# Performance work log

Measured on AMD Instinct MI355X. Metric: run time of the kernel, lower is better.

The kernel has to match this reference:

```python
import jax, jax.numpy as jnp
import numpy as np
from jax.ops import segment_sum, segment_max

N = 100000   # nodes
E = 1600000  # edges
B = 256      # graphs
H = 128      # hidden_channels
F_IN = 4     # input_size
EPS = 1e-5


def _graph_norm(x, w, b, ms, batch):
    # PyG GraphNorm: out = w * (x - ms*mean_g) / sqrt(var_g + eps) + b
    cnt = jnp.maximum(segment_sum(jnp.ones((x.shape[0],), x.dtype), batch, num_segments=B), 1.0)
    mean = segment_sum(x, batch, num_segments=B) / cnt[:, None]
    out = x - mean[batch] * ms
    var = segment_sum(out * out, batch, num_segments=B) / cnt[:, None]
    return w * out / jnp.sqrt(var + EPS)[batch] + b


def _gcn(x, W, b, src, dst):
    # GCNConv with self-loops and symmetric normalization (src/dst already include self-loops)
    h = x @ W                                              # [N, H]
    deg = segment_sum(jnp.ones_like(src, dtype=h.dtype), dst, num_segments=N)
    dinv = jax.lax.rsqrt(jnp.maximum(deg, 1.0))
    norm = dinv[src] * dinv[dst]                           # [E+N]
    return segment_sum(norm[:, None] * h[src], dst, num_segments=N) + b


def _seg_softmax(gate, batch):
    gmax = segment_max(gate, batch, num_segments=B)
    e = jnp.exp(gate - gmax[batch])
    den = segment_sum(e, batch, num_segments=B)
    return e / den[batch]


def setup_inputs() -> dict:
    key = jax.random.key(0)
    ks = jax.random.split(key, 16)
    x = jax.random.normal(ks[0], (N, F_IN), jnp.float32)
    edge_index = jax.random.randint(ks[1], (2, E), 0, N, dtype=jnp.int64)
    batch = jnp.sort(jax.random.randint(ks[2], (N,), 0, B, dtype=jnp.int64))
    r = lambda k, shp, fan: jax.random.normal(k, shp, jnp.float32) / np.sqrt(fan)
    inp = {
        "x": x, "edge_index": edge_index, "batch": batch,
        "W1": r(ks[3], (F_IN, H), F_IN), "b1": jnp.zeros((H,), jnp.float32),
        "W2": r(ks[4], (H, H), H), "b2": jnp.zeros((H,), jnp.float32),
        "W3": r(ks[5], (H, H), H), "b3": jnp.zeros((H,), jnp.float32),
        "gn0_w": jnp.ones((F_IN,), jnp.float32), "gn0_b": jnp.zeros((F_IN,), jnp.float32), "gn0_ms": jnp.ones((F_IN,), jnp.float32),
        "gn1_w": jnp.ones((H,), jnp.float32), "gn1_b": jnp.zeros((H,), jnp.float32), "gn1_ms": jnp.ones((H,), jnp.float32),
        "gn2_w": jnp.ones((H,), jnp.float32), "gn2_b": jnp.zeros((H,), jnp.float32), "gn2_ms": jnp.ones((H,), jnp.float32),
        "gn3_w": jnp.ones((H,), jnp.float32), "gn3_b": jnp.zeros((H,), jnp.float32), "gn3_ms": jnp.ones((H,), jnp.float32),
        "g1": r(ks[6], (H, H), H), "gb1": jnp.zeros((H,), jnp.float32),
        "g2": r(ks[7], (H, H), H), "gb2": jnp.zeros((H,), jnp.float32),
        "g3": r(ks[8], (H, 1), H), "gb3": jnp.zeros((1,), jnp.float32),
        "l1": r(ks[9], (H, H), H), "lb1": jnp.zeros((H,), jnp.float32),
        "l2": r(ks[10], (H, H), H), "lb2": jnp.zeros((H,), jnp.float32),
        "l3": r(ks[11], (H, 1), H), "lb3": jnp.zeros((1,), jnp.float32),
    }
    return inp


def reference(x, edge_index, batch, W1, b1, W2, b2, W3, b3,
              gn0_w, gn0_b, gn0_ms, gn1_w, gn1_b, gn1_ms,
              gn2_w, gn2_b, gn2_ms, gn3_w, gn3_b, gn3_ms,
              g1, gb1, g2, gb2, g3, gb3,
              l1, lb1, l2, lb2, l3, lb3):
    loop = jnp.arange(N, dtype=edge_index.dtype)
    src = jnp.concatenate([edge_index[0], loop])
    dst = jnp.concatenate([edge_index[1], loop])

    h = _graph_norm(x, gn0_w, gn0_b, gn0_ms, batch)
    h = _gcn(h, W1, b1, src, dst)
    h = jax.nn.relu(_graph_norm(h, gn1_w, gn1_b, gn1_ms, batch))
    h = _gcn(h, W2, b2, src, dst)
    h = jax.nn.relu(_graph_norm(h, gn2_w, gn2_b, gn2_ms, batch))
    h = _gcn(h, W3, b3, src, dst)
    h = _graph_norm(h, gn3_w, gn3_b, gn3_ms, batch)

    # GlobalAttention: gate_nn -> scalar gate per node, segment softmax, weighted sum
    g = jax.nn.relu(h @ g1 + gb1)
    g = jax.nn.relu(g @ g2 + gb2)
    gate = g @ g3 + gb3                                   # [N, 1]
    attn = _seg_softmax(gate, batch)                      # [N, 1]
    pooled = segment_sum(attn * h, batch, num_segments=B) # [B, H]

    o = jax.nn.relu(pooled @ l1 + lb1)
    o = jax.nn.relu(o @ l2 + lb2)
    return o @ l3 + lb3                                   # [B, 1]
```

## Files before the change

kernel.cpp:

```cpp
#include <hip/hip_runtime.h>
#include <hip/hip_bf16.h>

#define NN 100000
#define NE 1600000
#define NB 256
#define HD 128
#define EPS 1e-5f
#define NBUK 1563
#define SLOTB 1536
#define EPB 8192
#define NCHK 8

typedef __attribute__((ext_vector_type(8))) short bf16x8v;
typedef __attribute__((ext_vector_type(4))) float f32x4v;

__device__ __forceinline__ float rd_dyn(const void* p, int i, int fflag) {
    if (fflag) {
        unsigned short u = ((const unsigned short*)p)[i];
        return __uint_as_float(((unsigned)u) << 16);
    }
    return ((const float*)p)[i];
}

__device__ __forceinline__ int rd_idx(const int* p, int k, int iflag) {
    return iflag ? p[k] : p[2 * k];
}

__device__ __forceinline__ unsigned short f2bf(float v) {
    __hip_bfloat16 b = __float2bfloat16(v);
    return *(unsigned short*)&b;
}

__device__ __forceinline__ float bflo(unsigned u) { return __uint_as_float(u << 16); }
__device__ __forceinline__ float bfhi(unsigned u) { return __uint_as_float(u & 0xFFFF0000u); }
__device__ __forceinline__ unsigned packbf(float a, float b) {
    return (unsigned)f2bf(a) | ((unsigned)f2bf(b) << 16);
}

__global__ void k_mark7(unsigned short* __restrict__ out, int n) {
    int i = blockIdx.x * blockDim.x + threadIdx.x;
    if (i < n) out[i] = 0x40E0;
}

__global__ void k_init(const unsigned* __restrict__ w, int* __restrict__ flags) {
    if (threadIdx.x == 0 && blockIdx.x == 0) {
        flags[0] = 0;
        flags[1] = (w[0] == 0x3F803F80u) ? 1 : 0;
    }
}

__global__ void k_detect(const int* __restrict__ w, int* __restrict__ iflag, int n) {
    int i = blockIdx.x * blockDim.x + threadIdx.x;
    if (i < n && (i & 1) && w[i] != 0) atomicOr(iflag, 1);
}

struct CvtArgs {
    const void* p[30];
    int n[30];
    int off[30];
};
__global__ void k_cvtf_all(CvtArgs a, float* __restrict__ out, const int* __restrict__ fflagp) {
    int j = blockIdx.y;
    int i = blockIdx.x * blockDim.x + threadIdx.x;
    if (i >= a.n[j]) return;
    out[a.off[j] + i] = rd_dyn(a.p[j], i, *fflagp);
}

__global__ void k_transp(const float* __restrict__ P, int o0, int o1, int o2, int o3,
                         unsigned short* __restrict__ WT) {
    int mat = blockIdx.y;
    int off = mat == 0 ? o0 : mat == 1 ? o1 : mat == 2 ? o2 : o3;
    int i = blockIdx.x * 256 + threadIdx.x;
    int nidx = i >> 7, k = i & 127;
    WT[mat * 16384 + nidx * 128 + k] = f2bf(P[off + k * 128 + nidx]);
}

__global__ void k_start(const int* __restrict__ batch, const int* __restrict__ iflagp,
                        int* __restrict__ start, int* __restrict__ batch32,
                        int* __restrict__ bcur, int n) {
    int i = blockIdx.x * blockDim.x + threadIdx.x;
    if (i >= n) return;
    if (i < NBUK) bcur[i] = i * SLOTB;
    int ifl = *iflagp;
    int b = rd_idx(batch, i, ifl); b = b < 0 ? 0 : (b > NB - 1 ? NB - 1 : b);
    batch32[i] = b;
    int bp;
    if (i == 0) bp = -1;
    else { bp = rd_idx(batch, i - 1, ifl); bp = bp < 0 ? 0 : (bp > NB - 1 ? NB - 1 : bp); }
    for (int g = bp + 1; g <= b; ++g) start[g] = i;
    if (i == n - 1) { for (int g = b + 1; g <= NB; ++g) start[g] = n; }
}

__global__ __launch_bounds__(256) void k_bfill(const int* __restrict__ ei,
                                               const int* __restrict__ iflagp,
                                               int* __restrict__ bcur,
                                               unsigned* __restrict__ bkte, int e) {
    __shared__ int lh[NBUK];
    __shared__ int lbase[NBUK];
    int ifl = *iflagp;
    for (int b = threadIdx.x; b < NBUK; b += 256) lh[b] = 0;
    __syncthreads();
    int s0 = blockIdx.x * EPB;
    int s1 = s0 + EPB; if (s1 > e) s1 = e;
    for (int i = s0 + threadIdx.x; i < s1; i += 256) {
        int d = rd_idx(ei, NE + i, ifl);
        int s = rd_idx(ei, i, ifl);
        if ((unsigned)d < (unsigned)NN && (unsigned)s < (unsigned)NN)
            atomicAdd(&lh[d >> 6], 1);
    }
    __syncthreads();
    for (int b = threadIdx.x; b < NBUK; b += 256) {
        int c = lh[b];
        if (c) { lbase[b] = atomicAdd(&bcur[b], c); lh[b] = 0; }
    }
    __syncthreads();
    for (int i = s0 + threadIdx.x; i < s1; i += 256) {
        int d = rd_idx(ei, NE + i, ifl);
        int s = rd_idx(ei, i, ifl);
        if ((unsigned)d < (unsigned)NN && (unsigned)s < (unsigned)NN) {
            int b = d >> 6;
            int li = atomicAdd(&lh[b], 1);
            bkte[lbase[b] + li] = ((unsigned)s << 6) | (unsigned)(d & 63);
        }
    }
}

__global__ __launch_bounds__(256) void k_csrfin(const unsigned* __restrict__ bkte,
                                                const int* __restrict__ bcur,
                                                int* __restrict__ rowptr,
                                                int* __restrict__ cnt,
                                                float* __restrict__ dinv,
                                                int* __restrict__ esrc) {
    __shared__ int lc[64];
    __shared__ int lcur[64];
    int b = blockIdx.x, t = threadIdx.x;
    int base = b * 64;
    if (t < 64) lc[t] = 0;
    __syncthreads();
    int r0 = b * SLOTB, r1 = bcur[b];
    for (int j = r0 + t; j < r1; j += 256)
        atomicAdd(&lc[(int)(bkte[j] & 63u)], 1);
    __syncthreads();
    if (t < 64) {
        int v = lc[t];
        int inc = v;
#pragma unroll
        for (int off = 1; off < 64; off <<= 1) {
            int nv = __shfl_up(inc, off, 64);
            if (t >= off) inc += nv;
        }
        int ex = r0 + inc - v;
        lcur[t] = ex;
        int node = base + t;
        if (node < NN) {
            rowptr[node] = ex;
            cnt[node] = v;
            dinv[node] = rsqrtf((float)(v + 1));
        }
    }
    __syncthreads();
    for (int j = r0 + t; j < r1; j += 256) {
        unsigned p = bkte[j];
        int slot = atomicAdd(&lcur[p & 63u], 1);
        esrc[slot] = (int)(p >> 6);
    }
}

__global__ __launch_bounds__(64) void k_gn4(const void* __restrict__ x,
                                            const float* __restrict__ w,
                                            const float* __restrict__ bb,
                                            const float* __restrict__ ms,
                                            const int* __restrict__ start,
                                            const int* __restrict__ fflagp,
                                            float* __restrict__ out) {
    int g = blockIdx.x;
    int s0 = start[g], s1 = start[g + 1];
    if (s1 <= s0) return;
    int ff = *fflagp;
    float cnt = (float)(s1 - s0);
    int t = threadIdx.x;
    int c = t & 3, p = t >> 2;
    __shared__ float reds[64], redq[64];
    float s = 0.f, q = 0.f;
    for (int n = s0 + p; n < s1; n += 16) {
        float v = rd_dyn(x, n * 4 + c, ff);
        s += v; q = fmaf(v, v, q);
    }
    reds[t] = s; redq[t] = q; __syncthreads();
    for (int off = 8; off >= 1; off >>= 1) {
        if (p < off) { reds[t] += reds[t + 4 * off]; redq[t] += redq[t + 4 * off]; }
        __syncthreads();
    }
    float mean = reds[c] / cnt;
    float sq = redq[c] / cnt;
    float sub = mean * ms[c];
    float var = sq - 2.f * sub * mean + sub * sub;
    float scale = w[c] * rsqrtf(var + EPS);
    float bias = bb[c];
    for (int n = s0 + p; n < s1; n += 16) {
        float d = rd_dyn(x, n * 4 + c, ff) - sub;
        out[n * 4 + c] = scale * d + bias;
    }
}

__global__ __launch_bounds__(256) void k_gnstats_part(const unsigned* __restrict__ Xu,
                                                      const int* __restrict__ start,
                                                      float* __restrict__ PS,
                                                      float* __restrict__ PQ) {
    int g = blockIdx.x, k = blockIdx.y;
    int s0 = start[g], s1 = start[g + 1];
    int len = (s1 - s0 + NCHK - 1) / NCHK;
    int c0 = s0 + k * len, c1 = c0 + len; if (c1 > s1) c1 = s1;
    int t = threadIdx.x;
    int cp = t & 63, p = t >> 6;
    __shared__ float r0s[256], r1s[256], r0q[256], r1q[256];
    float s0a = 0.f, s1a = 0.f, q0a = 0.f, q1a = 0.f;
    for (int n = c0 + p; n < c1; n += 4) {
        unsigned u = Xu[n * 64 + cp];
        float lo = bflo(u), hi = bfhi(u);
        s0a += lo; q0a = fmaf(lo, lo, q0a);
        s1a += hi; q1a = fmaf(hi, hi, q1a);
    }
    r0s[t] = s0a; r1s[t] = s1a; r0q[t] = q0a; r1q[t] = q1a;
    __syncthreads();
    if (p == 0) {
        float a0 = r0s[cp] + r0s[64 + cp] + r0s[128 + cp] + r0s[192 + cp];
        float a1 = r1s[cp] + r1s[64 + cp] + r1s[128 + cp] + r1s[192 + cp];
        float b0 = r0q[cp] + r0q[64 + cp] + r0q[128 + cp] + r0q[192 + cp];
        float b1 = r1q[cp] + r1q[64 + cp] + r1q[128 + cp] + r1q[192 + cp];
        int bidx = (g * NCHK + k) * 128;
        PS[bidx + 2 * cp] = a0; PS[bidx + 2 * cp + 1] = a1;
        PQ[bidx + 2 * cp] = b0; PQ[bidx + 2 * cp + 1] = b1;
    }
}

__global__ __launch_bounds__(128) void k_gnstats_final(const float* __restrict__ PS,
                                                       const float* __restrict__ PQ,
                                                       const float* __restrict__ w,
                                                       const float* __restrict__ ms,
                                                       const int* __restrict__ start,
                                                       float* __restrict__ SUB,
                                                       float* __restrict__ SCALE) {
    int g = blockIdx.x, c = threadIdx.x;
    int n = start[g + 1] - start[g];
    if (n <= 0) return;
    float cnt = (float)n;
    float s = 0.f, q = 0.f;
#pragma unroll
    for (int k = 0; k < NCHK; ++k) {
        s += PS[(g * NCHK + k) * 128 + c];
        q += PQ[(g * NCHK + k) * 128 + c];
    }
    float mean = s / cnt;
    float sq = q / cnt;
    float sub = mean * ms[c];
    float var = sq - 2.f * sub * mean + sub * sub;
    SUB[g * 128 + c] = sub;
    SCALE[g * 128 + c] = w[c] * rsqrtf(var + EPS);
}

__global__ __launch_bounds__(256) void k_gather4gemm(const int* __restrict__ rowptr,
                                                     const int* __restrict__ cnt,
                                                     const int* __restrict__ esrc,
                                                     const float* __restrict__ dinv,
                                                     const float* __restrict__ h0,
                                                     const float* __restrict__ W1,
                                                     const float* __restrict__ b1,
                                                     unsigned* __restrict__ Xu) {
    __shared__ float w1s[512];
    __shared__ float b1s[128];
    int tid = threadIdx.x;
    w1s[tid] = W1[tid];
    w1s[256 + tid] = W1[256 + tid];
    if (tid < 128) b1s[tid] = b1[tid];
    __syncthreads();
    int node = blockIdx.x * 4 + (tid >> 6);
    int lane = tid & 63;
    if (node >= NN) return;
    int ch = lane & 3;
    int r0 = rowptr[node], r1 = r0 + cnt[node];
    float acc = 0.f;
    for (int j = r0 + (lane >> 2); j < r1; j += 16) {
        int s = esrc[j];
        acc += dinv[s] * h0[s * 4 + ch];
    }
#pragma unroll
    for (int mask = 4; mask <= 32; mask <<= 1)
        acc += __shfl_xor(acc, mask, 64);
    float dd = dinv[node];
    float z = dd * acc + dd * dd * h0[node * 4 + ch];
    float za = __shfl(z, 0, 64), zb = __shfl(z, 1, 64);
    float zc = __shfl(z, 2, 64), zd = __shfl(z, 3, 64);
    int c0 = 2 * lane, c1 = 2 * lane + 1;
    float v0 = za * w1s[c0] + zb * w1s[128 + c0] + zc * w1s[256 + c0] + zd * w1s[384 + c0] + b1s[c0];
    float v1 = za * w1s[c1] + zb * w1s[128 + c1] + zc * w1s[256 + c1] + zd * w1s[384 + c1] + b1s[c1];
    Xu[node * 64 + lane] = packbf(v0, v1);
}

__global__ __launch_bounds__(256) void k_gemm_mfma_bf(const unsigned* __restrict__ Xu,
                                                      const int* __restrict__ batch32,
                                                      const float* __restrict__ SUB,
                                                      const float* __restrict__ SCALE,
                                                      const float* __restrict__ gnb,
                                                      int relu,
                                                      const unsigned short* __restrict__ WT,
                                                      const float* __restrict__ dinv,
                                                      unsigned short* __restrict__ out) {
    __shared__ unsigned short xs[16][136];
    int base = blockIdx.x * 16;
    int tid = threadIdx.x;
    for (int idx = tid; idx < 1024; idx += 256) {
        int r = idx >> 6, cp = idx & 63;
        int g = batch32[base + r];
        unsigned u = Xu[(base + r) * 64 + cp];
        float2 sub = ((const float2*)(SUB + g * 128))[cp];
        float2 sc  = ((const float2*)(SCALE + g * 128))[cp];
        float2 gb  = ((const float2*)gnb)[cp];
        float va = (bflo(u) - sub.x) * sc.x + gb.x;
        float vb = (bfhi(u) - sub.y) * sc.y + gb.y;
        if (relu) { va = fmaxf(va, 0.f); vb = fmaxf(vb, 0.f); }
        xs[r][2 * cp] = f2bf(va);
        xs[r][2 * cp + 1] = f2bf(vb);
    }
    __syncthreads();
    int wave = tid >> 6, lane = tid & 63;
    int m = lane & 15, quad = lane >> 4;
    f32x4v acc0 = {0.f, 0.f, 0.f, 0.f}, acc1 = {0.f, 0.f, 0.f, 0.f};
    int c0 = wave * 32 + m, c1 = c0 + 16;
#pragma unroll
    for (int kk = 0; kk < 4; ++kk) {
        int ko = kk * 32 + quad * 8;
        bf16x8v a  = *(const bf16x8v*)&xs[m][ko];
        bf16x8v b0 = *(const bf16x8v*)&WT[c0 * 128 + ko];
        bf16x8v b1 = *(const bf16x8v*)&WT[c1 * 128 + ko];
        acc0 = __builtin_amdgcn_mfma_f32_16x16x32_bf16(a, b0, acc0, 0, 0, 0);
        acc1 = __builtin_amdgcn_mfma_f32_16x16x32_bf16(a, b1, acc1, 0, 0, 0);
    }
#pragma unroll
    for (int reg = 0; reg < 4; ++reg) {
        int row = base + quad * 4 + reg;
        float dv = dinv[row];
        out[row * 128 + c0] = f2bf(dv * acc0[reg]);
        out[row * 128 + c1] = f2bf(dv * acc1[reg]);
    }
}

#define ACC4(u) do { \
    a0 += bflo((u).x); a1 += bfhi((u).x); \
    a2 += bflo((u).y); a3 += bfhi((u).y); \
    a4 += bflo((u).z); a5 += bfhi((u).z); \
    a6 += bflo((u).w); a7 += bfhi((u).w); } while (0)

__global__ __launch_bounds__(256) void k_gather_bf(const int* __restrict__ rowptr,
                                                   const int* __restrict__ cnt,
                                                   const int* __restrict__ esrc,
                                                   const float* __restrict__ dinv,
                                                   const unsigned* __restrict__ h,
                                                   const float* __restrict__ bias,
                                                   unsigned* __restrict__ Xu) {
    int node = blockIdx.x * 4 + (threadIdx.x >> 6);
    int lane = threadIdx.x & 63;
    if (node >= NN) return;
    int q = lane >> 4, s = lane & 15;
    int r0 = rowptr[node], r1 = r0 + cnt[node];
    const uint4* hp = (const uint4*)h;
    float a0 = 0.f, a1 = 0.f, a2 = 0.f, a3 = 0.f;
    float a4 = 0.f, a5 = 0.f, a6 = 0.f, a7 = 0.f;
    int j = r0 + q;
    for (; j + 12 < r1; j += 16) {
        int e0 = esrc[j], e1 = esrc[j + 4], e2 = esrc[j + 8], e3 = esrc[j + 12];
        uint4 u0 = hp[e0 * 16 + s];
        uint4 u1 = hp[e1 * 16 + s];
        uint4 u2 = hp[e2 * 16 + s];
        uint4 u3 = hp[e3 * 16 + s];
        ACC4(u0); ACC4(u1); ACC4(u2); ACC4(u3);
    }
    for (; j + 4 < r1; j += 8) {
        int e0 = esrc[j], e1 = esrc[j + 4];
        uint4 u0 = hp[e0 * 16 + s];
        uint4 u1 = hp[e1 * 16 + s];
        ACC4(u0); ACC4(u1);
    }
    for (; j < r1; j += 4) {
        int e0 = esrc[j];
        uint4 u0 = hp[e0 * 16 + s];
        ACC4(u0);
    }
    a0 += __shfl_xor(a0, 16, 64); a0 += __shfl_xor(a0, 32, 64);
    a1 += __shfl_xor(a1, 16, 64); a1 += __shfl_xor(a1, 32, 64);
    a2 += __shfl_xor(a2, 16, 64); a2 += __shfl_xor(a2, 32, 64);
    a3 += __shfl_xor(a3, 16, 64); a3 += __shfl_xor(a3, 32, 64);
    a4 += __shfl_xor(a4, 16, 64); a4 += __shfl_xor(a4, 32, 64);
    a5 += __shfl_xor(a5, 16, 64); a5 += __shfl_xor(a5, 32, 64);
    a6 += __shfl_xor(a6, 16, 64); a6 += __shfl_xor(a6, 32, 64);
    a7 += __shfl_xor(a7, 16, 64); a7 += __shfl_xor(a7, 32, 64);
    int cp = 4 * s + q;
    float ax = q == 0 ? a0 : q == 1 ? a2 : q == 2 ? a4 : a6;
    float ay = q == 0 ? a1 : q == 1 ? a3 : q == 2 ? a5 : a7;
    float dd = dinv[node];
    unsigned us = h[node * 64 + cp];
    float2 bb = ((const float2*)bias)[cp];
    float ox = dd * (ax + bflo(us)) + bb.x;
    float oy = dd * (ay + bfhi(us)) + bb.y;
    Xu[node * 64 + cp] = packbf(ox, oy);
}

__global__ __launch_bounds__(256) void k_gate_fused(const unsigned* __restrict__ Xu,
                                                    const int* __restrict__ batch32,
                                                    const float* __restrict__ SUB,
                                                    const float* __restrict__ SCALE,
                                                    const float* __restrict__ gnb,
                                                    const unsigned short* __restrict__ GT1,
                                                    const float* __restrict__ gb1,
                                                    const unsigned short* __restrict__ GT2,
                                                    const float* __restrict__ gb2,
                                                    const float* __restrict__ g3,
                                                    const float* __restrict__ gb3,
                                                    float* __restrict__ gate) {
    __shared__ unsigned short xs[16][136];
    __shared__ unsigned short t1[16][136];
    __shared__ float redw[64];
    int base = blockIdx.x * 16;
    int tid = threadIdx.x;
    for (int idx = tid; idx < 1024; idx += 256) {
        int r = idx >> 6, cp = idx & 63;
        int g = batch32[base + r];
        unsigned u = Xu[(base + r) * 64 + cp];
        float2 sub = ((const float2*)(SUB + g * 128))[cp];
        float2 sc  = ((const float2*)(SCALE + g * 128))[cp];
        float2 gb  = ((const float2*)gnb)[cp];
        xs[r][2 * cp] = f2bf((bflo(u) - sub.x) * sc.x + gb.x);
        xs[r][2 * cp + 1] = f2bf((bfhi(u) - sub.y) * sc.y + gb.y);
    }
    __syncthreads();
    int wave = tid >> 6, lane = tid & 63;
    int m = lane & 15, quad = lane >> 4;
    int c0 = wave * 32 + m, c1 = c0 + 16;
    f32x4v acc0 = {0.f, 0.f, 0.f, 0.f}, acc1 = {0.f, 0.f, 0.f, 0.f};
#pragma unroll
    for (int kk = 0; kk < 4; ++kk) {
        int ko = kk * 32 + quad * 8;
        bf16x8v a  = *(const bf16x8v*)&xs[m][ko];
        bf16x8v b0 = *(const bf16x8v*)&GT1[c0 * 128 + ko];
        bf16x8v b1 = *(const bf16x8v*)&GT1[c1 * 128 + ko];
        acc0 = __builtin_amdgcn_mfma_f32_16x16x32_bf16(a, b0, acc0, 0, 0, 0);
        acc1 = __builtin_amdgcn_mfma_f32_16x16x32_bf16(a, b1, acc1, 0, 0, 0);
    }
    float bj0 = gb1[c0], bj1 = gb1[c1];
#pragma unroll
    for (int reg = 0; reg < 4; ++reg) {
        int row = quad * 4 + reg;
        t1[row][c0] = f2bf(fmaxf(acc0[reg] + bj0, 0.f));
        t1[row][c1] = f2bf(fmaxf(acc1[reg] + bj1, 0.f));
    }
    __syncthreads();
    f32x4v d0 = {0.f, 0.f, 0.f, 0.f}, d1 = {0.f, 0.f, 0.f, 0.f};
#pragma unroll
    for (int kk = 0; kk < 4; ++kk) {
        int ko = kk * 32 + quad * 8;
        bf16x8v a  = *(const bf16x8v*)&t1[m][ko];
        bf16x8v b0 = *(const bf16x8v*)&GT2[c0 * 128 + ko];
        bf16x8v b1 = *(const bf16x8v*)&GT2[c1 * 128 + ko];
        d0 = __builtin_amdgcn_mfma_f32_16x16x32_bf16(a, b0, d0, 0, 0, 0);
        d1 = __builtin_amdgcn_mfma_f32_16x16x32_bf16(a, b1, d1, 0, 0, 0);
    }
    float g30 = g3[c0], g31 = g3[c1];
    float bk0 = gb2[c0], bk1 = gb2[c1];
    float contrib[4];
#pragma unroll
    for (int reg = 0; reg < 4; ++reg) {
        float v0 = fmaxf(d0[reg] + bk0, 0.f);
        float v1 = fmaxf(d1[reg] + bk1, 0.f);
        contrib[reg] = v0 * g30 + v1 * g31;
    }
#pragma unroll
    for (int mask = 1; mask <= 8; mask <<= 1) {
#pragma unroll
        for (int reg = 0; reg < 4; ++reg)
            contrib[reg] += __shfl_xor(contrib[reg], mask, 64);
    }
    if (m == 0) {
#pragma unroll
        for (int reg = 0; reg < 4; ++reg)
            redw[wave * 16 + quad * 4 + reg] = contrib[reg];
    }
    __syncthreads();
    if (tid < 16) {
        float s = redw[tid] + redw[16 + tid] + redw[32 + tid] + redw[48 + tid];
        gate[base + tid] = s + gb3[0];
    }
}

__global__ __launch_bounds__(256) void k_smstats(const float* __restrict__ gate,
                                                 const int* __restrict__ start,
                                                 float2* __restrict__ SM) {
    int g = blockIdx.x;
    int s0 = start[g], s1 = start[g + 1];
    int t = threadIdx.x;
    __shared__ float red[256];
    if (s1 <= s0) { if (t == 0) SM[g] = make_float2(0.f, 1.f); return; }
    float m = -1e30f;
    for (int i = s0 + t; i < s1; i += 256) m = fmaxf(m, gate[i]);
    red[t] = m; __syncthreads();
    for (int off = 128; off; off >>= 1) { if (t < off) red[t] = fmaxf(red[t], red[t + off]); __syncthreads(); }
    m = red[0]; __syncthreads();
    float s = 0.f;
    for (int i = s0 + t; i < s1; i += 256) s += expf(gate[i] - m);
    red[t] = s; __syncthreads();
    for (int off = 128; off; off >>= 1) { if (t < off) red[t] += red[t + off]; __syncthreads(); }
    if (t == 0) SM[g] = make_float2(m, red[0]);
}

__global__ __launch_bounds__(256) void k_pool_part(const unsigned* __restrict__ Xu,
                                                   const float* __restrict__ SUB,
                                                   const float* __restrict__ SCALE,
                                                   const float* __restrict__ gnb,
                                                   const float* __restrict__ gate,
                                                   const float2* __restrict__ SM,
                                                   const int* __restrict__ start,
                                                   float* __restrict__ PP) {
    int g = blockIdx.x, k = blockIdx.y;
    int s0 = start[g], s1 = start[g + 1];
    int len = (s1 - s0 + NCHK - 1) / NCHK;
    int c0 = s0 + k * len, c1 = c0 + len; if (c1 > s1) c1 = s1;
    int t = threadIdx.x, cp = t & 63, p = t >> 6;
    __shared__ float r0s[256], r1s[256];
    float2 sm = SM[g];
    float invden = 1.f / sm.y;
    float2 sub = ((const float2*)(SUB + g * 128))[cp];
    float2 sc  = ((const float2*)(SCALE + g * 128))[cp];
    float2 gb  = ((const float2*)gnb)[cp];
    float sa = 0.f, sb = 0.f;
    for (int n = c0 + p; n < c1; n += 4) {
        float a = expf(gate[n] - sm.x) * invden;
        unsigned u = Xu[n * 64 + cp];
        sa += a * ((bflo(u) - sub.x) * sc.x + gb.x);
        sb += a * ((bfhi(u) - sub.y) * sc.y + gb.y);
    }
    r0s[t] = sa; r1s[t] = sb; __syncthreads();
    if (p == 0) {
        int bidx = (g * NCHK + k) * 128;
        float2 o;
        o.x = r0s[cp] + r0s[64 + cp] + r0s[128 + cp] + r0s[192 + cp];
        o.y = r1s[cp] + r1s[64 + cp] + r1s[128 + cp] + r1s[192 + cp];
        ((float2*)(PP + bidx))[cp] = o;
    }
}

__global__ __launch_bounds__(128) void k_head(const float* __restrict__ PP,
                                              const float* __restrict__ l1, const float* __restrict__ lb1,
                                              const float* __restrict__ l2, const float* __restrict__ lb2,
                                              const float* __restrict__ l3, const float* __restrict__ lb3,
                                              const int* __restrict__ fflagp,
                                              void* __restrict__ out) {
    int g = blockIdx.x, t = threadIdx.x;
    __shared__ float p[128], o[128], red[128];
    float s = 0.f;
#pragma unroll
    for (int k = 0; k < NCHK; ++k) s += PP[(g * NCHK + k) * 128 + t];
    p[t] = s; __syncthreads();
    float a = 0.f;
    for (int k = 0; k < 128; ++k) a += p[k] * l1[k * 128 + t];
    a = fmaxf(a + lb1[t], 0.f);
    o[t] = a; __syncthreads();
    float b = 0.f;
    for (int k = 0; k < 128; ++k) b += o[k] * l2[k * 128 + t];
    b = fmaxf(b + lb2[t], 0.f);
    red[t] = b * l3[t]; __syncthreads();
    for (int off = 64; off; off >>= 1) { if (t < off) red[t] += red[t + off]; __syncthreads(); }
    if (t == 0) {
        float r = red[0] + lb3[0];
        if (*fflagp) ((__hip_bfloat16*)out)[g] = __float2bfloat16(r);
        else ((float*)out)[g] = r;
    }
}

extern "C" void kernel_launch(void* const* d_in, const int* in_sizes, int n_in,
                              void* d_out, int out_size, void* d_ws, size_t ws_size,
                              hipStream_t stream) {
    const void* x = d_in[0];
    const int* ei_raw = (const int*)d_in[1];
    const int* batch_raw = (const int*)d_in[2];
    (void)n_in; (void)out_size;

    char* ws = (char*)d_ws;
    size_t off = 0;
    auto alloc = [&](size_t bytes) -> void* {
        void* p = ws + off;
        off += (bytes + 255) & ~(size_t)255;
        return p;
    };
    unsigned* Xu  = (unsigned*)alloc((size_t)NN * HD * 2);
    float* Y      = (float*)alloc((size_t)NN * HD * 4);
    float* h0     = (float*)alloc((size_t)NN * 4 * 4);
    float* dinv   = (float*)alloc((size_t)NN * 4);
    float* gate   = (float*)alloc((size_t)NN * 4);
    int*   start  = (int*)alloc((size_t)(NB + 1) * 4);
    int*   batch32= (int*)alloc((size_t)NN * 4);
    float* P      = (float*)alloc((size_t)131072 * 4);
    unsigned short* WT = (unsigned short*)alloc((size_t)4 * 16384 * 2);
    float* SUB    = (float*)alloc((size_t)NB * HD * 4);
    float* SCALE  = (float*)alloc((size_t)NB * HD * 4);
    float* PS     = (float*)alloc((size_t)NB * NCHK * 128 * 4);
    float* PQ     = (float*)alloc((size_t)NB * NCHK * 128 * 4);
    float2* SM    = (float2*)alloc((size_t)NB * 8);
    int*   flags  = (int*)alloc(256);
    int*   rowptr = (int*)alloc((size_t)NN * 4);
    int*   cnt    = (int*)alloc((size_t)NN * 4);
    int*   esrc   = (int*)alloc((size_t)NBUK * SLOTB * 4);
    int*   bcur   = (int*)alloc((size_t)NBUK * 4);
    unsigned* bkte = (unsigned*)(Y + (size_t)NN * HD / 2);
    float* PP = PS;

    if (ws_size < off) {
        k_mark7<<<1, 256, 0, stream>>>((unsigned short*)d_out, NB);
        return;
    }

    int* iflag = flags;
    int* fflag = flags + 1;
    k_init<<<1, 64, 0, stream>>>((const unsigned*)d_in[12], flags);
    k_detect<<<(NN + 255) / 256, 256, 0, stream>>>(batch_raw, iflag, NN);

    CvtArgs ca;
    float* fp[33];
    int maxn = 1;
    {
        int poff = 0;
        for (int i = 3; i < 33; ++i) {
            int n = in_sizes[i];
            ca.p[i - 3] = d_in[i];
            ca.n[i - 3] = n;
            ca.off[i - 3] = poff;
            fp[i] = P + poff;
            poff += n;
            if (n > maxn) maxn = n;
        }
    }
    {
        dim3 grid((maxn + 255) / 256, 30);
        k_cvtf_all<<<grid, 256, 0, stream>>>(ca, P, fflag);
    }
    const float *W1 = fp[3], *b1 = fp[4], *b2 = fp[6], *b3 = fp[8];
    const float *gn0w = fp[9],  *gn0b = fp[10], *gn0m = fp[11];
    const float *gn1w = fp[12], *gn1b = fp[13], *gn1m = fp[14];
    const float *gn2w = fp[15], *gn2b = fp[16], *gn2m = fp[17];
    const float *gn3w = fp[18], *gn3b = fp[19], *gn3m = fp[20];
    const float *gb1 = fp[22], *gb2 = fp[24], *g3 = fp[25], *gb3 = fp[26];
    const float *l1 = fp[27], *lb1 = fp[28], *l2 = fp[29], *lb2 = fp[30], *l3 = fp[31], *lb3 = fp[32];

    {
        dim3 grid(64, 4);
        k_transp<<<grid, 256, 0, stream>>>(P, (int)(fp[5] - P), (int)(fp[7] - P),
                                           (int)(fp[21] - P), (int)(fp[23] - P), WT);
    }
    const unsigned short* WT2 = WT;
    const unsigned short* WT3 = WT + 16384;
    const unsigned short* GT1 = WT + 2 * 16384;
    const unsigned short* GT2 = WT + 3 * 16384;

    k_start<<<(NN + 255) / 256, 256, 0, stream>>>(batch_raw, iflag, start, batch32, bcur, NN);

    int ebg = (NE + EPB - 1) / EPB;
    k_bfill<<<ebg, 256, 0, stream>>>(ei_raw, iflag, bcur, bkte, NE);
    k_csrfin<<<NBUK, 256, 0, stream>>>(bkte, bcur, rowptr, cnt, dinv, esrc);

    k_gn4<<<NB, 64, 0, stream>>>(x, gn0w, gn0b, gn0m, start, fflag, h0);

    k_gather4gemm<<<(NN + 3) / 4, 256, 0, stream>>>(rowptr, cnt, esrc, dinv, h0, W1, b1, Xu);

    unsigned short* Yb = (unsigned short*)Y;
    dim3 sgrid(NB, NCHK);

    k_gnstats_part<<<sgrid, 256, 0, stream>>>(Xu, start, PS, PQ);
    k_gnstats_final<<<NB, 128, 0, stream>>>(PS, PQ, gn1w, gn1m, start, SUB, SCALE);
    k_gemm_mfma_bf<<<NN / 16, 256, 0, stream>>>(Xu, batch32, SUB, SCALE, gn1b, 1, WT2, dinv, Yb);
    k_gather_bf<<<(NN + 3) / 4, 256, 0, stream>>>(rowptr, cnt, esrc, dinv, (const unsigned*)Yb, b2, Xu);

    k_gnstats_part<<<sgrid, 256, 0, stream>>>(Xu, start, PS, PQ);
    k_gnstats_final<<<NB, 128, 0, stream>>>(PS, PQ, gn2w, gn2m, start, SUB, SCALE);
    k_gemm_mfma_bf<<<NN / 16, 256, 0, stream>>>(Xu, batch32, SUB, SCALE, gn2b, 1, WT3, dinv, Yb);
    k_gather_bf<<<(NN + 3) / 4, 256, 0, stream>>>(rowptr, cnt, esrc, dinv, (const unsigned*)Yb, b3, Xu);

    k_gnstats_part<<<sgrid, 256, 0, stream>>>(Xu, start, PS, PQ);
    k_gnstats_final<<<NB, 128, 0, stream>>>(PS, PQ, gn3w, gn3m, start, SUB, SCALE);
    k_gate_fused<<<NN / 16, 256, 0, stream>>>(Xu, batch32, SUB, SCALE, gn3b,
                                              GT1, gb1, GT2, gb2, g3, gb3, gate);
    k_smstats<<<NB, 256, 0, stream>>>(gate, start, SM);
    k_pool_part<<<sgrid, 256, 0, stream>>>(Xu, SUB, SCALE, gn3b, gate, SM, start, PP);
    k_head<<<NB, 128, 0, stream>>>(PP, l1, lb1, l2, lb2, l3, lb3, fflag, d_out);
}
```

Measured before the change: 540.1 us.

## Merge small setup kernels, vectorize GraphNorm-0 and layer-1 gather, fuse softmax into pooling

Folds the flag-init kernel into the detect kernel (with a memset) and the weight transpose into the parameter-convert kernel. The pooling kernel now also computes the per-graph softmax max and denominator, so the separate stats kernel goes away; each chunk block recomputes those graph-wide stats redundantly. The input GraphNorm and the first gather switch to float4 per-node loads with one node per lane, and the GraphNorm block grows to 256 threads. The goal is fewer launches and better memory coalescing, at the cost of some duplicated reduction work.

```diff
diff --git a/kernel.cpp b/kernel.cpp
--- a/kernel.cpp
+++ b/kernel.cpp
@@ -42,37 +42,34 @@
     if (i < n) out[i] = 0x40E0;
 }
 
-__global__ void k_init(const unsigned* __restrict__ w, int* __restrict__ flags) {
-    if (threadIdx.x == 0 && blockIdx.x == 0) {
-        flags[0] = 0;
-        flags[1] = (w[0] == 0x3F803F80u) ? 1 : 0;
-    }
-}
-
-__global__ void k_detect(const int* __restrict__ w, int* __restrict__ iflag, int n) {
+__global__ void k_detect(const int* __restrict__ batch, const unsigned* __restrict__ w,
+                         int* __restrict__ flags, int n) {
     int i = blockIdx.x * blockDim.x + threadIdx.x;
-    if (i < n && (i & 1) && w[i] != 0) atomicOr(iflag, 1);
+    if (i == 0 && w[0] == 0x3F803F80u) atomicOr(&flags[1], 1);
+    if (i < n && (i & 1) && batch[i] != 0) atomicOr(&flags[0], 1);
 }
 
 struct CvtArgs {
     const void* p[30];
     int n[30];
     int off[30];
+    const void* wp[4];
 };
-__global__ void k_cvtf_all(CvtArgs a, float* __restrict__ out, const int* __restrict__ fflagp) {
+__global__ void k_cvtf_all(CvtArgs a, float* __restrict__ out,
+                           unsigned short* __restrict__ WT,
+                           const int* __restrict__ fflagp) {
     int j = blockIdx.y;
     int i = blockIdx.x * blockDim.x + threadIdx.x;
-    if (i >= a.n[j]) return;
-    out[a.off[j] + i] = rd_dyn(a.p[j], i, *fflagp);
-}
-
-__global__ void k_transp(const float* __restrict__ P, int o0, int o1, int o2, int o3,
-                         unsigned short* __restrict__ WT) {
-    int mat = blockIdx.y;
-    int off = mat == 0 ? o0 : mat == 1 ? o1 : mat == 2 ? o2 : o3;
-    int i = blockIdx.x * 256 + threadIdx.x;
-    int nidx = i >> 7, k = i & 127;
-    WT[mat * 16384 + nidx * 128 + k] = f2bf(P[off + k * 128 + nidx]);
+    int ff = *fflagp;
+    if (j < 30) {
+        if (i >= a.n[j]) return;
+        out[a.off[j] + i] = rd_dyn(a.p[j], i, ff);
+    } else {
+        int mat = j - 30;
+        if (i >= 16384) return;
+        int nidx = i >> 7, k = i & 127;
+        WT[mat * 16384 + nidx * 128 + k] = f2bf(rd_dyn(a.wp[mat], k * 128 + nidx, ff));
+    }
 }
 
 __global__ void k_start(const int* __restrict__ batch, const int* __restrict__ iflagp,
@@ -166,40 +163,72 @@
     }
 }
 
-__global__ __launch_bounds__(64) void k_gn4(const void* __restrict__ x,
-                                            const float* __restrict__ w,
-                                            const float* __restrict__ bb,
-                                            const float* __restrict__ ms,
-                                            const int* __restrict__ start,
-                                            const int* __restrict__ fflagp,
-                                            float* __restrict__ out) {
+__global__ __launch_bounds__(256) void k_gn4(const void* __restrict__ x,
+                                             const float* __restrict__ w,
+                                             const float* __restrict__ bb,
+                                             const float* __restrict__ ms,
+                                             const int* __restrict__ start,
+                                             const int* __restrict__ fflagp,
+                                             float* __restrict__ out) {
     int g = blockIdx.x;
     int s0 = start[g], s1 = start[g + 1];
     if (s1 <= s0) return;
     int ff = *fflagp;
     float cnt = (float)(s1 - s0);
     int t = threadIdx.x;
-    int c = t & 3, p = t >> 2;
-    __shared__ float reds[64], redq[64];
-    float s = 0.f, q = 0.f;
-    for (int n = s0 + p; n < s1; n += 16) {
-        float v = rd_dyn(x, n * 4 + c, ff);
-        s += v; q = fmaf(v, v, q);
-    }
-    reds[t] = s; redq[t] = q; __syncthreads();
-    for (int off = 8; off >= 1; off >>= 1) {
-        if (p < off) { reds[t] += reds[t + 4 * off]; redq[t] += redq[t + 4 * off]; }
+    __shared__ float4 rs[256], rq[256];
+    float sx = 0.f, sy = 0.f, sz = 0.f, sw = 0.f;
+    float qx = 0.f, qy = 0.f, qz = 0.f, qw = 0.f;
+    for (int n = s0 + t; n < s1; n += 256) {
+        float4 v;
+        if (ff) {
+            uint2 u = ((const uint2*)x)[n];
+            v.x = bflo(u.x); v.y = bfhi(u.x); v.z = bflo(u.y); v.w = bfhi(u.y);
+        } else {
+            v = ((const float4*)x)[n];
+        }
+        sx += v.x; sy += v.y; sz += v.z; sw += v.w;
+        qx = fmaf(v.x, v.x, qx); qy = fmaf(v.y, v.y, qy);
+        qz = fmaf(v.z, v.z, qz); qw = fmaf(v.w, v.w, qw);
+    }
+    rs[t] = make_float4(sx, sy, sz, sw);
+    rq[t] = make_float4(qx, qy, qz, qw);
+    __syncthreads();
+    for (int off = 128; off; off >>= 1) {
+        if (t < off) {
+            rs[t].x += rs[t + off].x; rs[t].y += rs[t + off].y;
+            rs[t].z += rs[t + off].z; rs[t].w += rs[t + off].w;
+            rq[t].x += rq[t + off].x; rq[t].y += rq[t + off].y;
+            rq[t].z += rq[t + off].z; rq[t].w += rq[t + off].w;
+        }
         __syncthreads();
     }
-    float mean = reds[c] / cnt;
-    float sq = redq[c] / cnt;
-    float sub = mean * ms[c];
-    float var = sq - 2.f * sub * mean + sub * sub;
-    float scale = w[c] * rsqrtf(var + EPS);
-    float bias = bb[c];
-    for (int n = s0 + p; n < s1; n += 16) {
-        float d = rd_dyn(x, n * 4 + c, ff) - sub;
-        out[n * 4 + c] = scale * d + bias;
+    float4 S = rs[0], Q = rq[0];
+    float4 wv = ((const float4*)w)[0];
+    float4 bv = ((const float4*)bb)[0];
+    float4 mv = ((const float4*)ms)[0];
+    float4 mean = make_float4(S.x / cnt, S.y / cnt, S.z / cnt, S.w / cnt);
+    float4 sub = make_float4(mean.x * mv.x, mean.y * mv.y, mean.z * mv.z, mean.w * mv.w);
+    float4 scale;
+    scale.x = wv.x * rsqrtf(Q.x / cnt - 2.f * sub.x * mean.x + sub.x * sub.x + EPS);
+    scale.y = wv.y * rsqrtf(Q.y / cnt - 2.f * sub.y * mean.y + sub.y * sub.y + EPS);
+    scale.z = wv.z * rsqrtf(Q.z / cnt - 2.f * sub.z * mean.z + sub.z * sub.z + EPS);
+    scale.w = wv.w * rsqrtf(Q.w / cnt - 2.f * sub.w * mean.w + sub.w * sub.w + EPS);
+    float4* op = (float4*)out;
+    for (int n = s0 + t; n < s1; n += 256) {
+        float4 v;
+        if (ff) {
+            uint2 u = ((const uint2*)x)[n];
+            v.x = bflo(u.x); v.y = bfhi(u.x); v.z = bflo(u.y); v.w = bfhi(u.y);
+        } else {
+            v = ((const float4*)x)[n];
+        }
+        float4 o;
+        o.x = scale.x * (v.x - sub.x) + bv.x;
+        o.y = scale.y * (v.y - sub.y) + bv.y;
+        o.z = scale.z * (v.z - sub.z) + bv.z;
+        o.w = scale.w * (v.w - sub.w) + bv.w;
+        op[n] = o;
     }
 }
 
@@ -277,20 +306,27 @@
     int node = blockIdx.x * 4 + (tid >> 6);
     int lane = tid & 63;
     if (node >= NN) return;
-    int ch = lane & 3;
     int r0 = rowptr[node], r1 = r0 + cnt[node];
-    float acc = 0.f;
-    for (int j = r0 + (lane >> 2); j < r1; j += 16) {
+    const float4* h4 = (const float4*)h0;
+    float ax = 0.f, ay = 0.f, az = 0.f, aw = 0.f;
+    for (int j = r0 + lane; j < r1; j += 64) {
         int s = esrc[j];
-        acc += dinv[s] * h0[s * 4 + ch];
-    }
-#pragma unroll
-    for (int mask = 4; mask <= 32; mask <<= 1)
-        acc += __shfl_xor(acc, mask, 64);
+        float dv = dinv[s];
+        float4 h = h4[s];
+        ax = fmaf(dv, h.x, ax); ay = fmaf(dv, h.y, ay);
+        az = fmaf(dv, h.z, az); aw = fmaf(dv, h.w, aw);
+    }
+#pragma unroll
+    for (int mask = 1; mask <= 32; mask <<= 1) {
+        ax += __shfl_xor(ax, mask, 64); ay += __shfl_xor(ay, mask, 64);
+        az += __shfl_xor(az, mask, 64); aw += __shfl_xor(aw, mask, 64);
+    }
     float dd = dinv[node];
-    float z = dd * acc + dd * dd * h0[node * 4 + ch];
-    float za = __shfl(z, 0, 64), zb = __shfl(z, 1, 64);
-    float zc = __shfl(z, 2, 64), zd = __shfl(z, 3, 64);
+    float4 hn = h4[node];
+    float za = dd * ax + dd * dd * hn.x;
+    float zb = dd * ay + dd * dd * hn.y;
+    float zc = dd * az + dd * dd * hn.z;
+    float zd = dd * aw + dd * dd * hn.w;
     int c0 = 2 * lane, c1 = 2 * lane + 1;
     float v0 = za * w1s[c0] + zb * w1s[128 + c0] + zc * w1s[256 + c0] + zd * w1s[384 + c0] + b1s[c0];
     float v1 = za * w1s[c1] + zb * w1s[128 + c1] + zc * w1s[256 + c1] + zd * w1s[384 + c1] + b1s[c1];
@@ -491,55 +527,51 @@
     }
 }
 
-__global__ __launch_bounds__(256) void k_smstats(const float* __restrict__ gate,
-                                                 const int* __restrict__ start,
-                                                 float2* __restrict__ SM) {
-    int g = blockIdx.x;
+__global__ __launch_bounds__(256) void k_smpool(const unsigned* __restrict__ Xu,
+                                                const float* __restrict__ SUB,
+                                                const float* __restrict__ SCALE,
+                                                const float* __restrict__ gnb,
+                                                const float* __restrict__ gate,
+                                                const int* __restrict__ start,
+                                                float* __restrict__ PP) {
+    int g = blockIdx.x, kk = blockIdx.y;
     int s0 = start[g], s1 = start[g + 1];
     int t = threadIdx.x;
     __shared__ float red[256];
-    if (s1 <= s0) { if (t == 0) SM[g] = make_float2(0.f, 1.f); return; }
+    __shared__ float r0s[256], r1s[256];
+    if (s1 <= s0) {
+        if (t < 64) {
+            int bidx = (g * NCHK + kk) * 128;
+            ((float2*)(PP + bidx))[t] = make_float2(0.f, 0.f);
+        }
+        return;
+    }
     float m = -1e30f;
     for (int i = s0 + t; i < s1; i += 256) m = fmaxf(m, gate[i]);
     red[t] = m; __syncthreads();
     for (int off = 128; off; off >>= 1) { if (t < off) red[t] = fmaxf(red[t], red[t + off]); __syncthreads(); }
     m = red[0]; __syncthreads();
-    float s = 0.f;
-    for (int i = s0 + t; i < s1; i += 256) s += expf(gate[i] - m);
-    red[t] = s; __syncthreads();
+    float sden = 0.f;
+    for (int i = s0 + t; i < s1; i += 256) sden += expf(gate[i] - m);
+    red[t] = sden; __syncthreads();
     for (int off = 128; off; off >>= 1) { if (t < off) red[t] += red[t + off]; __syncthreads(); }
-    if (t == 0) SM[g] = make_float2(m, red[0]);
-}
-
-__global__ __launch_bounds__(256) void k_pool_part(const unsigned* __restrict__ Xu,
-                                                   const float* __restrict__ SUB,
-                                                   const float* __restrict__ SCALE,
-                                                   const float* __restrict__ gnb,
-                                                   const float* __restrict__ gate,
-                                                   const float2* __restrict__ SM,
-                                                   const int* __restrict__ start,
-                                                   float* __restrict__ PP) {
-    int g = blockIdx.x, k = blockIdx.y;
-    int s0 = start[g], s1 = start[g + 1];
+    float invden = 1.f / red[0];
     int len = (s1 - s0 + NCHK - 1) / NCHK;
-    int c0 = s0 + k * len, c1 = c0 + len; if (c1 > s1) c1 = s1;
-    int t = threadIdx.x, cp = t & 63, p = t >> 6;
-    __shared__ float r0s[256], r1s[256];
-    float2 sm = SM[g];
-    float invden = 1.f / sm.y;
+    int c0 = s0 + kk * len, c1 = c0 + len; if (c1 > s1) c1 = s1;
+    int cp = t & 63, p = t >> 6;
     float2 sub = ((const float2*)(SUB + g * 128))[cp];
     float2 sc  = ((const float2*)(SCALE + g * 128))[cp];
     float2 gb  = ((const float2*)gnb)[cp];
     float sa = 0.f, sb = 0.f;
     for (int n = c0 + p; n < c1; n += 4) {
-        float a = expf(gate[n] - sm.x) * invden;
+        float a = expf(gate[n] - m) * invden;
         unsigned u = Xu[n * 64 + cp];
         sa += a * ((bflo(u) - sub.x) * sc.x + gb.x);
         sb += a * ((bfhi(u) - sub.y) * sc.y + gb.y);
     }
     r0s[t] = sa; r1s[t] = sb; __syncthreads();
     if (p == 0) {
-        int bidx = (g * NCHK + k) * 128;
+        int bidx = (g * NCHK + kk) * 128;
         float2 o;
         o.x = r0s[cp] + r0s[64 + cp] + r0s[128 + cp] + r0s[192 + cp];
         o.y = r1s[cp] + r1s[64 + cp] + r1s[128 + cp] + r1s[192 + cp];
@@ -603,7 +635,6 @@
     float* SCALE  = (float*)alloc((size_t)NB * HD * 4);
     float* PS     = (float*)alloc((size_t)NB * NCHK * 128 * 4);
     float* PQ     = (float*)alloc((size_t)NB * NCHK * 128 * 4);
-    float2* SM    = (float2*)alloc((size_t)NB * 8);
     int*   flags  = (int*)alloc(256);
     int*   rowptr = (int*)alloc((size_t)NN * 4);
     int*   cnt    = (int*)alloc((size_t)NN * 4);
@@ -619,12 +650,12 @@
 
     int* iflag = flags;
     int* fflag = flags + 1;
-    k_init<<<1, 64, 0, stream>>>((const unsigned*)d_in[12], flags);
-    k_detect<<<(NN + 255) / 256, 256, 0, stream>>>(batch_raw, iflag, NN);
+    hipMemsetAsync(flags, 0, 8, stream);
+    k_detect<<<(NN + 255) / 256, 256, 0, stream>>>(batch_raw, (const unsigned*)d_in[12], flags, NN);
 
     CvtArgs ca;
     float* fp[33];
-    int maxn = 1;
+    int maxn = 16384;
     {
         int poff = 0;
         for (int i = 3; i < 33; ++i) {
@@ -636,10 +667,14 @@
             poff += n;
             if (n > maxn) maxn = n;
         }
+        ca.wp[0] = d_in[5];
+        ca.wp[1] = d_in[7];
+        ca.wp[2] = d_in[21];
+        ca.wp[3] = d_in[23];
     }
     {
-        dim3 grid((maxn + 255) / 256, 30);
-        k_cvtf_all<<<grid, 256, 0, stream>>>(ca, P, fflag);
+        dim3 grid((maxn + 255) / 256, 34);
+        k_cvtf_all<<<grid, 256, 0, stream>>>(ca, P, WT, fflag);
     }
     const float *W1 = fp[3], *b1 = fp[4], *b2 = fp[6], *b3 = fp[8];
     const float *gn0w = fp[9],  *gn0b = fp[10], *gn0m = fp[11];
@@ -649,11 +684,6 @@
     const float *gb1 = fp[22], *gb2 = fp[24], *g3 = fp[25], *gb3 = fp[26];
     const float *l1 = fp[27], *lb1 = fp[28], *l2 = fp[29], *lb2 = fp[30], *l3 = fp[31], *lb3 = fp[32];
 
-    {
-        dim3 grid(64, 4);
-        k_transp<<<grid, 256, 0, stream>>>(P, (int)(fp[5] - P), (int)(fp[7] - P),
-                                           (int)(fp[21] - P), (int)(fp[23] - P), WT);
-    }
     const unsigned short* WT2 = WT;
     const unsigned short* WT3 = WT + 16384;
     const unsigned short* GT1 = WT + 2 * 16384;
@@ -665,7 +695,7 @@
     k_bfill<<<ebg, 256, 0, stream>>>(ei_raw, iflag, bcur, bkte, NE);
     k_csrfin<<<NBUK, 256, 0, stream>>>(bkte, bcur, rowptr, cnt, dinv, esrc);
 
-    k_gn4<<<NB, 64, 0, stream>>>(x, gn0w, gn0b, gn0m, start, fflag, h0);
+    k_gn4<<<NB, 256, 0, stream>>>(x, gn0w, gn0b, gn0m, start, fflag, h0);
 
     k_gather4gemm<<<(NN + 3) / 4, 256, 0, stream>>>(rowptr, cnt, esrc, dinv, h0, W1, b1, Xu);
 
@@ -686,7 +716,6 @@
     k_gnstats_final<<<NB, 128, 0, stream>>>(PS, PQ, gn3w, gn3m, start, SUB, SCALE);
     k_gate_fused<<<NN / 16, 256, 0, stream>>>(Xu, batch32, SUB, SCALE, gn3b,
                                               GT1, gb1, GT2, gb2, g3, gb3, gate);
-    k_smstats<<<NB, 256, 0, stream>>>(gate, start, SM);
-    k_pool_part<<<sgrid, 256, 0, stream>>>(Xu, SUB, SCALE, gn3b, gate, SM, start, PP);
+    k_smpool<<<sgrid, 256, 0, stream>>>(Xu, SUB, SCALE, gn3b, gate, start, PP);
     k_head<<<NB, 128, 0, stream>>>(PP, l1, lb1, l2, lb2, l3, lb3, fflag, d_out);
 }
```

Measured after the change: 532.7 us. No clear change (-1.4%).
